# Optimization experiments

Measured on AMD Instinct MI355X. Metric: run time of the kernel, lower is better.

## Reference

```python
import jax, jax.numpy as jnp
import numpy as np

N = 100_000   # entities
E = 1_000_000 # edges (triples)
R = 1_000     # relations
D = 100       # node_hidden
DEPTH = 2
EPS = 1e-12


def _segment_mean(vals, idx, num):
    s = jax.ops.segment_sum(vals, idx, num_segments=num)
    cnt = jax.ops.segment_sum(jnp.ones((vals.shape[0],), vals.dtype), idx, num_segments=num)
    return s / jnp.maximum(cnt, 1.0)[:, None]


def _edge_softmax(logits, dst, num):
    # softmax over edges grouped by destination node
    m = jax.ops.segment_max(logits, dst, num_segments=num)
    e = jnp.exp(logits - m[dst])
    s = jax.ops.segment_sum(e, dst, num_segments=num)
    return e / s[dst]


def _rrea_encoder(features, rel_emb, src, dst, erel, kernels):
    feats = jnp.tanh(features)
    outs = [feats]
    for l in range(DEPTH):
        rels = rel_emb[erel]                                        # [E, D]
        rels = rels / jnp.maximum(jnp.linalg.norm(rels, axis=1, keepdims=True), EPS)
        neighs = feats[src]                                         # [E, D]
        selfs = feats[dst]                                          # [E, D]
        # Householder reflection of neighbor features about relation direction
        neighs = neighs - 2.0 * jnp.sum(neighs * rels, axis=1, keepdims=True) * rels
        k = kernels[l]                                              # [3D, 1]
        w_s, w_n, w_r = k[:D, 0], k[D:2 * D, 0], k[2 * D:, 0]
        logits = selfs @ w_s + neighs @ w_n + rels @ w_r            # [E]
        att = _edge_softmax(logits, dst, N)
        feats = jax.ops.segment_sum(neighs * att[:, None], dst, num_segments=N)
        feats = jnp.tanh(feats)
        outs.append(feats)
    return jnp.concatenate(outs, axis=1)                            # [N, (DEPTH+1)*D]


def setup_inputs() -> dict:
    key = jax.random.key(0)
    k1, k2, k3, k4, k5, k6, k7 = jax.random.split(key, 7)
    ent_emb = jax.random.uniform(k1, (N, D), jnp.float32, -0.05, 0.05)
    rel_emb = jax.random.uniform(k2, (R, D), jnp.float32, -0.05, 0.05)
    attn_e = jax.random.normal(k3, (DEPTH, 3 * D, 1), jnp.float32)
    attn_r = jax.random.normal(k4, (DEPTH, 3 * D, 1), jnp.float32)
    src = jax.random.randint(k5, (E,), 0, N, jnp.int32)
    dst = jnp.sort(jax.random.randint(k6, (E,), 0, N, jnp.int32))
    erel = jax.random.randint(k7, (E,), 0, R, jnp.int32)
    return {"ent_emb": ent_emb, "rel_emb": rel_emb, "attn_e": attn_e,
            "attn_r": attn_r, "src": src, "dst": dst, "erel": erel}


def reference(ent_emb, rel_emb, attn_e, attn_r, src, dst, erel):
    # initial entity feature: mean of in-neighbor entity embeddings
    ent_feature = _segment_mean(ent_emb[src], dst, N)               # [N, D]
    # initial relation feature per entity: mean of incident relation embeddings
    rel_feature = _segment_mean(rel_emb[erel], dst, N)              # [N, D]
    out_ent = _rrea_encoder(ent_feature, rel_emb, src, dst, erel, attn_e)
    out_rel = _rrea_encoder(rel_feature, rel_emb, src, dst, erel, attn_r)
    # dropout_rate=0.0 / eval mode -> identity
    return jnp.concatenate([out_ent, out_rel], axis=-1)             # [N, 2*(DEPTH+1)*D]
```

## Files before the change

### kernel.cpp

```cpp
#include <hip/hip_runtime.h>
#include <hip/hip_fp16.h>
#include <math.h>

#define NN 100000
#define NE 1000000
#define NR 1000
#define DD 100
#define HS 104
#define FS2 208
#define OUTC 600
#define EPS 1e-12f
#define NBIN 64
#define RESCALE_THR 8.0f
#define NWCH (NN / 16)

struct __attribute__((aligned(16))) h8 { unsigned short u[8]; };

__device__ inline float h2f(unsigned short u) {
    __half_raw r; r.x = u; __half h = r; return __half2float(h);
}
__device__ inline unsigned short f2h(float f) {
    __half h = __float2half_rn(f); __half_raw r = h; return r.x;
}

__device__ inline float wave_sum(float v) {
#pragma unroll
    for (int o = 32; o > 0; o >>= 1) v += __shfl_down(v, o, 64);
    return __shfl(v, 0, 64);
}
__device__ inline float quad_sum(float v) {
    v += __shfl_xor(v, 1, 64);
    v += __shfl_xor(v, 2, 64);
    return v;
}

__global__ void k_rowptr(const int* __restrict__ dst, int* __restrict__ row_ptr,
                         int* __restrict__ ghist) {
    int n = blockIdx.x * blockDim.x + threadIdx.x;
    if (n < NBIN) ghist[n] = 0;
    if (n > NN) return;
    int lo = 0, hi = NE;
    while (lo < hi) {
        int mid = (lo + hi) >> 1;
        if (dst[mid] < n) lo = mid + 1; else hi = mid;
    }
    row_ptr[n] = lo;
}

__global__ void k_hist(const int* __restrict__ row_ptr, int* __restrict__ ghist) {
    __shared__ int lh[NBIN];
    int t = threadIdx.x;
    if (t < NBIN) lh[t] = 0;
    __syncthreads();
    int n = blockIdx.x * blockDim.x + t;
    if (n < NN) {
        int d = row_ptr[n + 1] - row_ptr[n];
        atomicAdd(&lh[min(d, NBIN - 1)], 1);
    }
    __syncthreads();
    if (t < NBIN && lh[t]) atomicAdd(&ghist[t], lh[t]);
}
__global__ void k_scan(const int* __restrict__ ghist, int* __restrict__ goffs,
                       int* __restrict__ ctrs) {
    if (threadIdx.x == 0) {
        int s = 0;
        for (int i = 0; i < NBIN; ++i) { goffs[i] = s; s += ghist[i]; }
        ctrs[0] = 0; ctrs[1] = 0; ctrs[2] = 0;
    }
}
__global__ void k_scatter(const int* __restrict__ row_ptr, int* __restrict__ goffs,
                          int* __restrict__ perm) {
    __shared__ int lh[NBIN], base[NBIN];
    int t = threadIdx.x;
    if (t < NBIN) lh[t] = 0;
    __syncthreads();
    int n = blockIdx.x * blockDim.x + t;
    int bin = 0, rank = 0;
    if (n < NN) {
        int d = row_ptr[n + 1] - row_ptr[n];
        bin = min(d, NBIN - 1);
        rank = atomicAdd(&lh[bin], 1);
    }
    __syncthreads();
    if (t < NBIN && lh[t]) base[t] = atomicAdd(&goffs[t], lh[t]);
    __syncthreads();
    if (n < NN) perm[base[bin] + rank] = n;
}

__global__ void k_pack(const int* __restrict__ src, const int* __restrict__ erel,
                       unsigned int* __restrict__ ep) {
    int e = blockIdx.x * blockDim.x + threadIdx.x;
    if (e >= NE) return;
    ep[e] = (unsigned int)src[e] | ((unsigned int)erel[e] << 17);
}

__global__ void k_relnorm(const float* __restrict__ rel_emb, float* __restrict__ rel_norm,
                          unsigned short* __restrict__ rel_nh) {
    int w = (blockIdx.x * blockDim.x + threadIdx.x) >> 6;
    int lane = threadIdx.x & 63;
    if (w >= NR) return;
    const float* r = rel_emb + w * DD;
    float v0 = r[lane];
    float v1 = (lane + 64 < DD) ? r[lane + 64] : 0.f;
    float ss = wave_sum(v0 * v0 + v1 * v1);
    float sc = 1.f / fmaxf(sqrtf(ss), EPS);
    float* o = rel_norm + w * DD;
    unsigned short* oh = rel_nh + (size_t)w * HS;
    o[lane] = v0 * sc;
    oh[lane] = f2h(v0 * sc);
    if (lane + 64 < DD) {
        o[lane + 64] = v1 * sc;
        oh[lane + 64] = f2h(v1 * sc);
    }
}

__global__ void k_relv2(const float* __restrict__ rel_norm,
                        const float* __restrict__ k3dA, const float* __restrict__ k3dB,
                        float4* __restrict__ rrP) {
    int w = (blockIdx.x * blockDim.x + threadIdx.x) >> 6;
    int lane = threadIdx.x & 63;
    if (w >= NR) return;
    const float* r = rel_norm + w * DD;
    float r0 = r[lane];
    float r1 = (lane + 64 < DD) ? r[lane + 64] : 0.f;
    float wrA0 = k3dA[2 * DD + lane], wnA0 = k3dA[DD + lane];
    float wrB0 = k3dB[2 * DD + lane], wnB0 = k3dB[DD + lane];
    float wrA1 = 0.f, wnA1 = 0.f, wrB1 = 0.f, wnB1 = 0.f;
    if (lane + 64 < DD) {
        wrA1 = k3dA[2 * DD + lane + 64]; wnA1 = k3dA[DD + lane + 64];
        wrB1 = k3dB[2 * DD + lane + 64]; wnB1 = k3dB[DD + lane + 64];
    }
    float rdA = wave_sum(r0 * wrA0 + r1 * wrA1);
    float rdB = wave_sum(r0 * wrB0 + r1 * wrB1);
    float rnA = wave_sum(r0 * wnA0 + r1 * wnA1);
    float rnB = wave_sum(r0 * wnB0 + r1 * wnB1);
    if (lane == 0) { float4 v = { rdA, rdB, rnA, rnB }; rrP[w] = v; }
}

__global__ void k_tohalf(const float* __restrict__ s, unsigned short* __restrict__ d, int rows) {
    int gi = blockIdx.x * blockDim.x + threadIdx.x;
    int n = gi >> 2, sb = gi & 3;
    if (n >= rows) return;
    const float4* s4 = (const float4*)(s + (size_t)n * DD);
    unsigned short* dr = d + (size_t)n * HS;
#pragma unroll
    for (int j = 0; j < 3; ++j) {
        float4 a = s4[6 * sb + 2 * j];
        float4 b = s4[6 * sb + 2 * j + 1];
        h8 o;
        o.u[0] = f2h(a.x); o.u[1] = f2h(a.y); o.u[2] = f2h(a.z); o.u[3] = f2h(a.w);
        o.u[4] = f2h(b.x); o.u[5] = f2h(b.y); o.u[6] = f2h(b.z); o.u[7] = f2h(b.w);
        ((h8*)(dr + 24 * sb))[j] = o;
    }
    dr[96 + sb] = f2h(s[(size_t)n * DD + 96 + sb]);
}


__global__ __launch_bounds__(256) void k_segmean2(
        const unsigned short* __restrict__ ent_h, const unsigned short* __restrict__ rel_eh,
        const unsigned int* __restrict__ ep,
        const int* __restrict__ row_ptr, const int* __restrict__ perm,
        const float* __restrict__ k3dA, const float* __restrict__ k3dB,
        float2* __restrict__ sdP, float2* __restrict__ ndP,
        unsigned short* __restrict__ fused_out,
        float* __restrict__ out, int* __restrict__ ctr) {
    int lane = threadIdx.x & 63;
    int qi = lane >> 2, sb = lane & 3;
    for (;;) {
        int t;
        if (lane == 0) t = atomicAdd(ctr, 1);
        t = __shfl(t, 0, 64);
        if (t >= NWCH) break;
        int gi = (NWCH - 1 - t) * 16 + qi;
        int n = perm[gi];
        int beg = row_ptr[n], end = row_ptr[n + 1];
        float a0[25] = {}, a1[25] = {};
        for (int e = beg; e < end; ++e) {
            unsigned int v = ep[e];
            int s = v & 0x1FFFF;
            int r = v >> 17;
            const unsigned short* er = ent_h + (size_t)s * HS;
            const unsigned short* rr = rel_eh + (size_t)r * HS;
            const h8* e8 = (const h8*)(er + 24 * sb);
            const h8* r8 = (const h8*)(rr + 24 * sb);
            h8 xa = e8[0], xb = e8[1], xc = e8[2];
            h8 ya = r8[0], yb = r8[1], yc = r8[2];
#pragma unroll
            for (int m = 0; m < 8; ++m) {
                a0[m]      += h2f(xa.u[m]);
                a0[8 + m]  += h2f(xb.u[m]);
                a0[16 + m] += h2f(xc.u[m]);
                a1[m]      += h2f(ya.u[m]);
                a1[8 + m]  += h2f(yb.u[m]);
                a1[16 + m] += h2f(yc.u[m]);
            }
            a0[24] += h2f(er[96 + sb]);
            a1[24] += h2f(rr[96 + sb]);
        }
        float inv = 1.f / fmaxf((float)(end - beg), 1.f);
        float o0[25], o1[25];
#pragma unroll
        for (int m = 0; m < 25; ++m) { o0[m] = tanhf(a0[m] * inv); o1[m] = tanhf(a1[m] * inv); }
        if (fused_out) {
            unsigned short* fr = fused_out + (size_t)n * FS2;
#pragma unroll
            for (int j = 0; j < 3; ++j) {
                h8 x, y;
#pragma unroll
                for (int m = 0; m < 8; ++m) { x.u[m] = f2h(o0[8 * j + m]); y.u[m] = f2h(o1[8 * j + m]); }
                ((h8*)(fr + 24 * sb))[j] = x;
                ((h8*)(fr + 104 + 24 * sb))[j] = y;
            }
            fr[96 + sb] = f2h(o0[24]);
            fr[200 + sb] = f2h(o1[24]);
        }
        float* oc = out + (size_t)n * OUTC;
        float4* oc4 = (float4*)oc;
        float4* od4 = (float4*)(oc + 300);
#pragma unroll
        for (int k = 0; k < 6; ++k) {
            float4 v0 = { o0[4 * k], o0[4 * k + 1], o0[4 * k + 2], o0[4 * k + 3] };
            oc4[6 * sb + k] = v0;
            float4 u0 = { o1[4 * k], o1[4 * k + 1], o1[4 * k + 2], o1[4 * k + 3] };
            od4[6 * sb + k] = u0;
        }
        oc[96 + sb] = o0[24];
        oc[300 + 96 + sb] = o1[24];
        float sp0 = o0[24] * k3dA[96 + sb], np0 = o0[24] * k3dA[DD + 96 + sb];
        float sp1 = o1[24] * k3dB[96 + sb], np1 = o1[24] * k3dB[DD + 96 + sb];
        const float4* wA = (const float4*)k3dA;
        const float4* wAn = (const float4*)(k3dA + DD);
        const float4* wB = (const float4*)k3dB;
        const float4* wBn = (const float4*)(k3dB + DD);
#pragma unroll
        for (int k = 0; k < 6; ++k) {
            float4 ws = wA[6 * sb + k], wn = wAn[6 * sb + k];
            sp0 += o0[4 * k] * ws.x + o0[4 * k + 1] * ws.y + o0[4 * k + 2] * ws.z + o0[4 * k + 3] * ws.w;
            np0 += o0[4 * k] * wn.x + o0[4 * k + 1] * wn.y + o0[4 * k + 2] * wn.z + o0[4 * k + 3] * wn.w;
            float4 vs = wB[6 * sb + k], vn = wBn[6 * sb + k];
            sp1 += o1[4 * k] * vs.x + o1[4 * k + 1] * vs.y + o1[4 * k + 2] * vs.z + o1[4 * k + 3] * vs.w;
            np1 += o1[4 * k] * vn.x + o1[4 * k + 1] * vn.y + o1[4 * k + 2] * vn.z + o1[4 * k + 3] * vn.w;
        }
        sp0 = quad_sum(sp0); np0 = quad_sum(np0);
        sp1 = quad_sum(sp1); np1 = quad_sum(np1);
        if (sb == 0) {
            float2 sv = { sp0, sp1 }; sdP[n] = sv;
            float2 nv = { np0, np1 }; ndP[n] = nv;
        }
    }
}

template<int SRC>
__global__ __launch_bounds__(256) void k_layer2(
        const void* __restrict__ Fin,
        const unsigned short* __restrict__ rel_nh,
        const unsigned int* __restrict__ ep,
        const int* __restrict__ row_ptr, const int* __restrict__ perm,
        const float2* __restrict__ sdP, const float2* __restrict__ ndP,
        const float4* __restrict__ rrP,
        const float* __restrict__ k3dA_next, const float* __restrict__ k3dB_next,
        float2* __restrict__ sdP_o, float2* __restrict__ ndP_o,
        unsigned short* __restrict__ fused_out,
        float* __restrict__ out, int ocol, int* __restrict__ ctr) {
    int lane = threadIdx.x & 63;
    int qi = lane >> 2, sb = lane & 3;
    for (;;) {
        int tk;
        if (lane == 0) tk = atomicAdd(ctr, 1);
        tk = __shfl(tk, 0, 64);
        if (tk >= NWCH) break;
        int gi = (NWCH - 1 - tk) * 16 + qi;
        int n = perm[gi];
        int beg = row_ptr[n], end = row_ptr[n + 1];
        float2 sd2 = sdP[n];
        float acc0[25] = {}, acc1[25] = {};
        float m0 = -INFINITY, l0 = 0.f, m1 = -INFINITY, l1 = 0.f;
        for (int e = beg; e < end; ++e) {
            unsigned int v = ep[e];
            int s = v & 0x1FFFF;
            int r = v >> 17;
            float2 nd2 = ndP[s];
            float4 rr = rrP[r];
            float f0[25], f1[25], rv[25];
            if (SRC == 0) {
                const unsigned short* fr = (const unsigned short*)Fin + (size_t)s * FS2;
                const h8* p = (const h8*)(fr + 24 * sb);
                const h8* q = (const h8*)(fr + 104 + 24 * sb);
                h8 x0 = p[0], x1 = p[1], x2 = p[2];
                h8 y0 = q[0], y1 = q[1], y2 = q[2];
#pragma unroll
                for (int m = 0; m < 8; ++m) {
                    f0[m] = h2f(x0.u[m]); f0[8 + m] = h2f(x1.u[m]); f0[16 + m] = h2f(x2.u[m]);
                    f1[m] = h2f(y0.u[m]); f1[8 + m] = h2f(y1.u[m]); f1[16 + m] = h2f(y2.u[m]);
                }
                f0[24] = h2f(fr[96 + sb]);
                f1[24] = h2f(fr[200 + sb]);
            } else {
                const float* fr = (const float*)Fin + (size_t)s * OUTC;
                const float4* a4 = (const float4*)fr;
                const float4* b4 = (const float4*)(fr + 300);
#pragma unroll
                for (int k = 0; k < 6; ++k) {
                    float4 vv = a4[6 * sb + k];
                    f0[4 * k] = vv.x; f0[4 * k + 1] = vv.y; f0[4 * k + 2] = vv.z; f0[4 * k + 3] = vv.w;
                    float4 uu = b4[6 * sb + k];
                    f1[4 * k] = uu.x; f1[4 * k + 1] = uu.y; f1[4 * k + 2] = uu.z; f1[4 * k + 3] = uu.w;
                }
                f0[24] = fr[96 + sb];
                f1[24] = fr[300 + 96 + sb];
            }
            const unsigned short* rh = rel_nh + (size_t)r * HS;
            const h8* rp = (const h8*)(rh + 24 * sb);
            h8 z0 = rp[0], z1 = rp[1], z2 = rp[2];
#pragma unroll
            for (int m = 0; m < 8; ++m) {
                rv[m] = h2f(z0.u[m]); rv[8 + m] = h2f(z1.u[m]); rv[16 + m] = h2f(z2.u[m]);
            }
            rv[24] = h2f(rh[96 + sb]);
            float p0 = f0[24] * rv[24], p1 = f1[24] * rv[24];
#pragma unroll
            for (int m = 0; m < 24; ++m) { p0 += f0[m] * rv[m]; p1 += f1[m] * rv[m]; }
            p0 = quad_sum(p0);
            p1 = quad_sum(p1);
            float c0 = 2.f * p0, c1 = 2.f * p1;
            float lg0 = sd2.x + nd2.x - c0 * rr.z + rr.x;
            float lg1 = sd2.y + nd2.y - c1 * rr.w + rr.y;
            float w0, w1;
            if (lg0 > m0 + RESCALE_THR) {
                float sc = __expf(m0 - lg0);
                l0 *= sc;
#pragma unroll
                for (int m = 0; m < 25; ++m) acc0[m] *= sc;
                m0 = lg0; w0 = 1.f;
            } else w0 = __expf(lg0 - m0);
            if (lg1 > m1 + RESCALE_THR) {
                float sc = __expf(m1 - lg1);
                l1 *= sc;
#pragma unroll
                for (int m = 0; m < 25; ++m) acc1[m] *= sc;
                m1 = lg1; w1 = 1.f;
            } else w1 = __expf(lg1 - m1);
            l0 += w0; l1 += w1;
            float wc0 = w0 * c0, wc1 = w1 * c1;
#pragma unroll
            for (int m = 0; m < 25; ++m) {
                acc0[m] += w0 * f0[m] - wc0 * rv[m];
                acc1[m] += w1 * f1[m] - wc1 * rv[m];
            }
        }
        float i0 = (end > beg) ? (1.f / l0) : 0.f;
        float i1 = (end > beg) ? (1.f / l1) : 0.f;
        float o0[25], o1[25];
#pragma unroll
        for (int m = 0; m < 25; ++m) { o0[m] = tanhf(acc0[m] * i0); o1[m] = tanhf(acc1[m] * i1); }
        if (fused_out) {
            unsigned short* fr = fused_out + (size_t)n * FS2;
#pragma unroll
            for (int j = 0; j < 3; ++j) {
                h8 x, y;
#pragma unroll
                for (int m = 0; m < 8; ++m) { x.u[m] = f2h(o0[8 * j + m]); y.u[m] = f2h(o1[8 * j + m]); }
                ((h8*)(fr + 24 * sb))[j] = x;
                ((h8*)(fr + 104 + 24 * sb))[j] = y;
            }
            fr[96 + sb] = f2h(o0[24]);
            fr[200 + sb] = f2h(o1[24]);
        }
        float* oc = out + (size_t)n * OUTC + ocol;
        float4* oc4 = (float4*)oc;
        float4* od4 = (float4*)(oc + 300);
#pragma unroll
        for (int k = 0; k < 6; ++k) {
            float4 vv = { o0[4 * k], o0[4 * k + 1], o0[4 * k + 2], o0[4 * k + 3] };
            oc4[6 * sb + k] = vv;
            float4 uu = { o1[4 * k], o1[4 * k + 1], o1[4 * k + 2], o1[4 * k + 3] };
            od4[6 * sb + k] = uu;
        }
        oc[96 + sb] = o0[24];
        oc[300 + 96 + sb] = o1[24];
        if (k3dA_next) {
            float sp0 = o0[24] * k3dA_next[96 + sb], np0 = o0[24] * k3dA_next[DD + 96 + sb];
            float sp1 = o1[24] * k3dB_next[96 + sb], np1 = o1[24] * k3dB_next[DD + 96 + sb];
            const float4* wA = (const float4*)k3dA_next;
            const float4* wAn = (const float4*)(k3dA_next + DD);
            const float4* wB = (const float4*)k3dB_next;
            const float4* wBn = (const float4*)(k3dB_next + DD);
#pragma unroll
            for (int k = 0; k < 6; ++k) {
                float4 ws = wA[6 * sb + k], wn = wAn[6 * sb + k];
                sp0 += o0[4 * k] * ws.x + o0[4 * k + 1] * ws.y + o0[4 * k + 2] * ws.z + o0[4 * k + 3] * ws.w;
                np0 += o0[4 * k] * wn.x + o0[4 * k + 1] * wn.y + o0[4 * k + 2] * wn.z + o0[4 * k + 3] * wn.w;
                float4 vs = wB[6 * sb + k], vn = wBn[6 * sb + k];
                sp1 += o1[4 * k] * vs.x + o1[4 * k + 1] * vs.y + o1[4 * k + 2] * vs.z + o1[4 * k + 3] * vs.w;
                np1 += o1[4 * k] * vn.x + o1[4 * k + 1] * vn.y + o1[4 * k + 2] * vn.z + o1[4 * k + 3] * vn.w;
            }
            sp0 = quad_sum(sp0); np0 = quad_sum(np0);
            sp1 = quad_sum(sp1); np1 = quad_sum(np1);
            if (sb == 0) {
                float2 sv = { sp0, sp1 }; sdP_o[n] = sv;
                float2 nv = { np0, np1 }; ndP_o[n] = nv;
            }
        }
    }
}

extern "C" void kernel_launch(void* const* d_in, const int* in_sizes, int n_in,
                              void* d_out, int out_size, void* d_ws, size_t ws_size,
                              hipStream_t stream) {
    const float* ent_emb = (const float*)d_in[0];
    const float* rel_emb = (const float*)d_in[1];
    const float* attn_e  = (const float*)d_in[2];
    const float* attn_r  = (const float*)d_in[3];
    const int*   src     = (const int*)d_in[4];
    const int*   dst     = (const int*)d_in[5];
    const int*   erel    = (const int*)d_in[6];
    float* out = (float*)d_out;

    char* ws = (char*)d_ws;
    auto al = [](size_t x) { return (x + 255) & ~(size_t)255; };
    size_t o = 0;
    auto take = [&](size_t bytes) -> void* { void* p = ws + o; o = al(o + bytes); return p; };

    int*    row_ptr = (int*)take((NN + 1) * sizeof(int));
    unsigned short* rel_nh = (unsigned short*)take((size_t)NR * HS * 2);
    float2* sdPA = (float2*)take(NN * sizeof(float2));
    float2* ndPA = (float2*)take(NN * sizeof(float2));
    float2* sdPB = (float2*)take(NN * sizeof(float2));
    float2* ndPB = (float2*)take(NN * sizeof(float2));
    float4* rrP0 = (float4*)take(NR * sizeof(float4));
    float4* rrP1 = (float4*)take(NR * sizeof(float4));
    int*    ghist = (int*)take(NBIN * sizeof(int));
    int*    goffs = (int*)take(NBIN * sizeof(int));
    int*    perm  = (int*)take(NN * sizeof(int));
    int*    ctrs  = (int*)take(3 * sizeof(int));
    unsigned int* ep = (unsigned int*)take((size_t)NE * 4);

    size_t tbl0 = o;
    size_t tbl1 = al(tbl0 + (size_t)NN * HS * 2);
    size_t tbl2 = al(tbl1 + (size_t)NR * HS * 2);
    size_t tblE = al(tbl2 + (size_t)NR * DD * 4);
    size_t fsz  = al((size_t)NN * FS2 * 2);
    size_t tblSpan = tblE - tbl0;
    size_t fA_A = tbl0 + (fsz > tblSpan ? fsz : tblSpan);
    bool planA = (fA_A + fsz) <= ws_size;
    size_t fA_off = planA ? fA_A : tblE;
    bool haveFA = planA || ((tblE + fsz) <= ws_size);

    unsigned short* ent_h  = (unsigned short*)(ws + tbl0);
    unsigned short* rel_eh = (unsigned short*)(ws + tbl1);
    float*          rel_norm = (float*)(ws + tbl2);
    unsigned short* fusedA = haveFA ? (unsigned short*)(ws + fA_off) : (unsigned short*)nullptr;
    unsigned short* fusedB = planA ? (unsigned short*)(ws + tbl0) : (unsigned short*)nullptr;

    hipLaunchKernelGGL(k_rowptr, dim3((NN + 256) / 256), dim3(256), 0, stream,
                       dst, row_ptr, ghist);
    hipLaunchKernelGGL(k_hist, dim3((NN + 255) / 256), dim3(256), 0, stream, row_ptr, ghist);
    hipLaunchKernelGGL(k_scan, dim3(1), dim3(64), 0, stream, ghist, goffs, ctrs);
    hipLaunchKernelGGL(k_scatter, dim3((NN + 255) / 256), dim3(256), 0, stream,
                       row_ptr, goffs, perm);
    hipLaunchKernelGGL(k_pack, dim3((NE + 255) / 256), dim3(256), 0, stream, src, erel, ep);
    hipLaunchKernelGGL(k_relnorm, dim3(NR * 64 / 256), dim3(256), 0, stream,
                       rel_emb, rel_norm, rel_nh);
    hipLaunchKernelGGL(k_relv2, dim3(NR * 64 / 256), dim3(256), 0, stream,
                       rel_norm, attn_e, attn_r, rrP0);
    hipLaunchKernelGGL(k_relv2, dim3(NR * 64 / 256), dim3(256), 0, stream,
                       rel_norm, attn_e + 300, attn_r + 300, rrP1);
    hipLaunchKernelGGL(k_tohalf, dim3((NN * 4 + 255) / 256), dim3(256), 0, stream,
                       ent_emb, ent_h, NN);
    hipLaunchKernelGGL(k_tohalf, dim3((NR * 4 + 255) / 256), dim3(256), 0, stream,
                       rel_emb, rel_eh, NR);

    hipLaunchKernelGGL(k_segmean2, dim3(2048), dim3(256), 0, stream,
                       ent_h, rel_eh, ep, row_ptr, perm,
                       attn_e, attn_r, sdPA, ndPA, fusedA, out, ctrs + 0);

    if (haveFA) {
        hipLaunchKernelGGL(HIP_KERNEL_NAME(k_layer2<0>), dim3(1024), dim3(256), 0, stream,
                           (const void*)fusedA, rel_nh, ep, row_ptr, perm,
                           sdPA, ndPA, rrP0, attn_e + 300, attn_r + 300,
                           sdPB, ndPB, fusedB, out, 100, ctrs + 1);
    } else {
        hipLaunchKernelGGL(HIP_KERNEL_NAME(k_layer2<1>), dim3(1024), dim3(256), 0, stream,
                           (const void*)out, rel_nh, ep, row_ptr, perm,
                           sdPA, ndPA, rrP0, attn_e + 300, attn_r + 300,
                           sdPB, ndPB, (unsigned short*)nullptr, out, 100, ctrs + 1);
    }

    if (planA) {
        hipLaunchKernelGGL(HIP_KERNEL_NAME(k_layer2<0>), dim3(1024), dim3(256), 0, stream,
                           (const void*)fusedB, rel_nh, ep, row_ptr, perm,
                           sdPB, ndPB, rrP1, (const float*)nullptr, (const float*)nullptr,
                           sdPB, ndPB, (unsigned short*)nullptr, out, 200, ctrs + 2);
    } else {
        hipLaunchKernelGGL(HIP_KERNEL_NAME(k_layer2<1>), dim3(1024), dim3(256), 0, stream,
                           (const void*)(out + 100), rel_nh, ep, row_ptr, perm,
                           sdPB, ndPB, rrP1, (const float*)nullptr, (const float*)nullptr,
                           sdPB, ndPB, (unsigned short*)nullptr, out, 200, ctrs + 2);
    }
}
```

Measured before the change: 883.0 us.

## Replace atomic work-stealing with static paired chunk assignment and unroll edge loop

The dynamic atomic counter scheduler in the segment-mean and layer kernels is replaced by a static mapping. Each wave processes one chunk of heavy-degree nodes and one mirrored chunk of light-degree nodes from the degree-sorted permutation to balance work. The grid becomes exactly enough waves for all pairs. The counters and their reset are removed. The segment-mean edge loop is also unrolled by two so more gathers are in flight, at the cost of more registers and possibly worse balance than dynamic stealing.

```diff
diff --git a/kernel.cpp b/kernel.cpp
--- a/kernel.cpp
+++ b/kernel.cpp
@@ -13,6 +13,8 @@
 #define NBIN 64
 #define RESCALE_THR 8.0f
 #define NWCH (NN / 16)
+#define NPAIR (NWCH / 2)
+#define GRID_HEAVY 782
 
 struct __attribute__((aligned(16))) h8 { unsigned short u[8]; };
 
@@ -60,12 +62,10 @@
     __syncthreads();
     if (t < NBIN && lh[t]) atomicAdd(&ghist[t], lh[t]);
 }
-__global__ void k_scan(const int* __restrict__ ghist, int* __restrict__ goffs,
-                       int* __restrict__ ctrs) {
+__global__ void k_scan(const int* __restrict__ ghist, int* __restrict__ goffs) {
     if (threadIdx.x == 0) {
         int s = 0;
         for (int i = 0; i < NBIN; ++i) { goffs[i] = s; s += ghist[i]; }
-        ctrs[0] = 0; ctrs[1] = 0; ctrs[2] = 0;
     }
 }
 __global__ void k_scatter(const int* __restrict__ row_ptr, int* __restrict__ goffs,
@@ -163,19 +163,48 @@
         const float* __restrict__ k3dA, const float* __restrict__ k3dB,
         float2* __restrict__ sdP, float2* __restrict__ ndP,
         unsigned short* __restrict__ fused_out,
-        float* __restrict__ out, int* __restrict__ ctr) {
+        float* __restrict__ out) {
+    int wv = (blockIdx.x * blockDim.x + threadIdx.x) >> 6;
     int lane = threadIdx.x & 63;
     int qi = lane >> 2, sb = lane & 3;
-    for (;;) {
-        int t;
-        if (lane == 0) t = atomicAdd(ctr, 1);
-        t = __shfl(t, 0, 64);
-        if (t >= NWCH) break;
-        int gi = (NWCH - 1 - t) * 16 + qi;
-        int n = perm[gi];
+    if (wv >= NPAIR) return;
+    for (int half = 0; half < 2; ++half) {
+        int c = half ? (NWCH - 1 - wv) : wv;
+        int n = perm[c * 16 + qi];
         int beg = row_ptr[n], end = row_ptr[n + 1];
         float a0[25] = {}, a1[25] = {};
-        for (int e = beg; e < end; ++e) {
+        int e = beg;
+        for (; e + 1 < end; e += 2) {
+            unsigned int v0 = ep[e], v1 = ep[e + 1];
+            int s0 = v0 & 0x1FFFF, r0 = v0 >> 17;
+            int s1 = v1 & 0x1FFFF, r1 = v1 >> 17;
+            const unsigned short* er0 = ent_h + (size_t)s0 * HS;
+            const unsigned short* rr0 = rel_eh + (size_t)r0 * HS;
+            const unsigned short* er1 = ent_h + (size_t)s1 * HS;
+            const unsigned short* rr1 = rel_eh + (size_t)r1 * HS;
+            const h8* pe0 = (const h8*)(er0 + 24 * sb);
+            const h8* pr0 = (const h8*)(rr0 + 24 * sb);
+            const h8* pe1 = (const h8*)(er1 + 24 * sb);
+            const h8* pr1 = (const h8*)(rr1 + 24 * sb);
+            h8 xa0 = pe0[0], xb0 = pe0[1], xc0 = pe0[2];
+            h8 ya0 = pr0[0], yb0 = pr0[1], yc0 = pr0[2];
+            h8 xa1 = pe1[0], xb1 = pe1[1], xc1 = pe1[2];
+            h8 ya1 = pr1[0], yb1 = pr1[1], yc1 = pr1[2];
+            unsigned short te0 = er0[96 + sb], tr0 = rr0[96 + sb];
+            unsigned short te1 = er1[96 + sb], tr1 = rr1[96 + sb];
+#pragma unroll
+            for (int m = 0; m < 8; ++m) {
+                a0[m]      += h2f(xa0.u[m]) + h2f(xa1.u[m]);
+                a0[8 + m]  += h2f(xb0.u[m]) + h2f(xb1.u[m]);
+                a0[16 + m] += h2f(xc0.u[m]) + h2f(xc1.u[m]);
+                a1[m]      += h2f(ya0.u[m]) + h2f(ya1.u[m]);
+                a1[8 + m]  += h2f(yb0.u[m]) + h2f(yb1.u[m]);
+                a1[16 + m] += h2f(yc0.u[m]) + h2f(yc1.u[m]);
+            }
+            a0[24] += h2f(te0) + h2f(te1);
+            a1[24] += h2f(tr0) + h2f(tr1);
+        }
+        if (e < end) {
             unsigned int v = ep[e];
             int s = v & 0x1FFFF;
             int r = v >> 17;
@@ -261,16 +290,14 @@
         const float* __restrict__ k3dA_next, const float* __restrict__ k3dB_next,
         float2* __restrict__ sdP_o, float2* __restrict__ ndP_o,
         unsigned short* __restrict__ fused_out,
-        float* __restrict__ out, int ocol, int* __restrict__ ctr) {
+        float* __restrict__ out, int ocol) {
+    int wv = (blockIdx.x * blockDim.x + threadIdx.x) >> 6;
     int lane = threadIdx.x & 63;
     int qi = lane >> 2, sb = lane & 3;
-    for (;;) {
-        int tk;
-        if (lane == 0) tk = atomicAdd(ctr, 1);
-        tk = __shfl(tk, 0, 64);
-        if (tk >= NWCH) break;
-        int gi = (NWCH - 1 - tk) * 16 + qi;
-        int n = perm[gi];
+    if (wv >= NPAIR) return;
+    for (int half = 0; half < 2; ++half) {
+        int c = half ? (NWCH - 1 - wv) : wv;
+        int n = perm[c * 16 + qi];
         int beg = row_ptr[n], end = row_ptr[n + 1];
         float2 sd2 = sdP[n];
         float acc0[25] = {}, acc1[25] = {};
@@ -432,7 +459,6 @@
     int*    ghist = (int*)take(NBIN * sizeof(int));
     int*    goffs = (int*)take(NBIN * sizeof(int));
     int*    perm  = (int*)take(NN * sizeof(int));
-    int*    ctrs  = (int*)take(3 * sizeof(int));
     unsigned int* ep = (unsigned int*)take((size_t)NE * 4);
 
     size_t tbl0 = o;
@@ -455,7 +481,7 @@
     hipLaunchKernelGGL(k_rowptr, dim3((NN + 256) / 256), dim3(256), 0, stream,
                        dst, row_ptr, ghist);
     hipLaunchKernelGGL(k_hist, dim3((NN + 255) / 256), dim3(256), 0, stream, row_ptr, ghist);
-    hipLaunchKernelGGL(k_scan, dim3(1), dim3(64), 0, stream, ghist, goffs, ctrs);
+    hipLaunchKernelGGL(k_scan, dim3(1), dim3(64), 0, stream, ghist, goffs);
     hipLaunchKernelGGL(k_scatter, dim3((NN + 255) / 256), dim3(256), 0, stream,
                        row_ptr, goffs, perm);
     hipLaunchKernelGGL(k_pack, dim3((NE + 255) / 256), dim3(256), 0, stream, src, erel, ep);
@@ -470,31 +496,31 @@
     hipLaunchKernelGGL(k_tohalf, dim3((NR * 4 + 255) / 256), dim3(256), 0, stream,
                        rel_emb, rel_eh, NR);
 
-    hipLaunchKernelGGL(k_segmean2, dim3(2048), dim3(256), 0, stream,
+    hipLaunchKernelGGL(k_segmean2, dim3(GRID_HEAVY), dim3(256), 0, stream,
                        ent_h, rel_eh, ep, row_ptr, perm,
-                       attn_e, attn_r, sdPA, ndPA, fusedA, out, ctrs + 0);
+                       attn_e, attn_r, sdPA, ndPA, fusedA, out);
 
     if (haveFA) {
-        hipLaunchKernelGGL(HIP_KERNEL_NAME(k_layer2<0>), dim3(1024), dim3(256), 0, stream,
+        hipLaunchKernelGGL(HIP_KERNEL_NAME(k_layer2<0>), dim3(GRID_HEAVY), dim3(256), 0, stream,
                            (const void*)fusedA, rel_nh, ep, row_ptr, perm,
                            sdPA, ndPA, rrP0, attn_e + 300, attn_r + 300,
-                           sdPB, ndPB, fusedB, out, 100, ctrs + 1);
+                           sdPB, ndPB, fusedB, out, 100);
     } else {
-        hipLaunchKernelGGL(HIP_KERNEL_NAME(k_layer2<1>), dim3(1024), dim3(256), 0, stream,
+        hipLaunchKernelGGL(HIP_KERNEL_NAME(k_layer2<1>), dim3(GRID_HEAVY), dim3(256), 0, stream,
                            (const void*)out, rel_nh, ep, row_ptr, perm,
                            sdPA, ndPA, rrP0, attn_e + 300, attn_r + 300,
-                           sdPB, ndPB, (unsigned short*)nullptr, out, 100, ctrs + 1);
+                           sdPB, ndPB, (unsigned short*)nullptr, out, 100);
     }
 
     if (planA) {
-        hipLaunchKernelGGL(HIP_KERNEL_NAME(k_layer2<0>), dim3(1024), dim3(256), 0, stream,
+        hipLaunchKernelGGL(HIP_KERNEL_NAME(k_layer2<0>), dim3(GRID_HEAVY), dim3(256), 0, stream,
                            (const void*)fusedB, rel_nh, ep, row_ptr, perm,
                            sdPB, ndPB, rrP1, (const float*)nullptr, (const float*)nullptr,
-                           sdPB, ndPB, (unsigned short*)nullptr, out, 200, ctrs + 2);
+                           sdPB, ndPB, (unsigned short*)nullptr, out, 200);
     } else {
-        hipLaunchKernelGGL(HIP_KERNEL_NAME(k_layer2<1>), dim3(1024), dim3(256), 0, stream,
+        hipLaunchKernelGGL(HIP_KERNEL_NAME(k_layer2<1>), dim3(GRID_HEAVY), dim3(256), 0, stream,
                            (const void*)(out + 100), rel_nh, ep, row_ptr, perm,
                            sdPB, ndPB, rrP1, (const float*)nullptr, (const float*)nullptr,
-                           sdPB, ndPB, (unsigned short*)nullptr, out, 200, ctrs + 2);
-    }
-}
+                           sdPB, ndPB, (unsigned short*)nullptr, out, 200);
+    }
+}
```

Result: faster. 738.6 us (-16.4%).
